# Kernel optimization log

Hardware: AMD Instinct MI355X
Metric: run time of the kernel (lower is better)

## Reference

```python
import jax, jax.numpy as jnp
import numpy as np

BETA = 0.25  # commitment_cost; use_ema=True path -> vq_loss = beta * mse(z_e, sg(z_q))


def setup_inputs() -> dict:
    key = jax.random.key(0)
    k1, k2 = jax.random.split(key)
    B, T, K, D = 8192, 16, 512, 128
    z_e = jax.random.normal(k1, (B, T, D), dtype=jnp.float32)
    # matches nn.init.uniform_(cb.weight, -1/K, 1/K), stacked over T slots
    codebooks = jax.random.uniform(k2, (T, K, D), dtype=jnp.float32,
                                   minval=-1.0 / K, maxval=1.0 / K)
    return {"z_e": z_e, "codebooks": codebooks}


def reference(z_e, codebooks):
    # z_e: (B, T, D); codebooks: (T, K, D)
    B, T, D = z_e.shape
    K = codebooks.shape[1]
    # per-slot squared distances: ||z||^2 - 2 z.w + ||w||^2 -> (B, T, K)
    distances = (jnp.sum(z_e * z_e, axis=-1, keepdims=True)
                 - 2.0 * jnp.einsum('btd,tkd->btk', z_e, codebooks)
                 + jnp.sum(codebooks * codebooks, axis=-1)[None, :, :])
    tokens = jnp.argmin(distances, axis=-1)          # (B, T) int
    # gather per-slot code vectors
    z_q = codebooks[jnp.arange(T)[None, :], tokens]  # (B, T, D)
    # straight-through estimator
    z_q_st = z_e + jax.lax.stop_gradient(z_q - z_e)
    # sum_t beta*mse_t / T == beta * mean over all elements (each slot mse is a B*D mean)
    vq_loss = BETA * jnp.mean(jnp.square(z_e - jax.lax.stop_gradient(z_q)))
    # utilization: total unique codes used per slot / (T*K)
    used = jnp.zeros((T, K), dtype=bool).at[jnp.arange(T)[None, :], tokens].set(True)
    utilization = jnp.sum(used).astype(jnp.float32) / (T * K)
    return z_q_st, tokens, vq_loss, utilization
```

## Files before the change

kernel.cpp:

```cpp
#include <hip/hip_runtime.h>
#include <cfloat>

#define TT 16
#define KK 512
#define DD 128
#define BSTRIPE 512
#define BC 32
#define NW 8
#define NCHUNK (BSTRIPE / BC)
#define N0 16777216
#define N1 131072
#define TAU 1e-4f

typedef _Float16 half8 __attribute__((ext_vector_type(8)));
typedef float f32x16 __attribute__((ext_vector_type(16)));

__device__ __forceinline__ float np_sum128_sq_f4(const float4* __restrict__ p) {
  float4 a = p[0], b = p[1];
  float r[8];
  r[0] = __fmul_rn(a.x, a.x); r[1] = __fmul_rn(a.y, a.y);
  r[2] = __fmul_rn(a.z, a.z); r[3] = __fmul_rn(a.w, a.w);
  r[4] = __fmul_rn(b.x, b.x); r[5] = __fmul_rn(b.y, b.y);
  r[6] = __fmul_rn(b.z, b.z); r[7] = __fmul_rn(b.w, b.w);
#pragma unroll
  for (int i = 1; i < 16; ++i) {
    a = p[2 * i]; b = p[2 * i + 1];
    r[0] = __fadd_rn(r[0], __fmul_rn(a.x, a.x));
    r[1] = __fadd_rn(r[1], __fmul_rn(a.y, a.y));
    r[2] = __fadd_rn(r[2], __fmul_rn(a.z, a.z));
    r[3] = __fadd_rn(r[3], __fmul_rn(a.w, a.w));
    r[4] = __fadd_rn(r[4], __fmul_rn(b.x, b.x));
    r[5] = __fadd_rn(r[5], __fmul_rn(b.y, b.y));
    r[6] = __fadd_rn(r[6], __fmul_rn(b.z, b.z));
    r[7] = __fadd_rn(r[7], __fmul_rn(b.w, b.w));
  }
  return __fadd_rn(__fadd_rn(__fadd_rn(r[0], r[1]), __fadd_rn(r[2], r[3])),
                   __fadd_rn(__fadd_rn(r[4], r[5]), __fadd_rn(r[6], r[7])));
}

__device__ __forceinline__ float dot128_chain(const float* __restrict__ zp,
                                              const float* __restrict__ cp) {
  float s = 0.0f;
#pragma unroll
  for (int d4 = 0; d4 < 32; ++d4) {
    const float4 a = *(const float4*)(zp + d4 * 4);
    const float4 c = *(const float4*)(cp + d4 * 4);
    s = __builtin_fmaf(a.x, c.x, s);
    s = __builtin_fmaf(a.y, c.y, s);
    s = __builtin_fmaf(a.z, c.z, s);
    s = __builtin_fmaf(a.w, c.w, s);
  }
  return s;
}

__device__ __forceinline__ void split8(const float4 a, const float4 b, const float sc,
                                       half8& h1, half8& h2) {
  const float v[8] = {a.x, a.y, a.z, a.w, b.x, b.y, b.z, b.w};
#pragma unroll
  for (int i = 0; i < 8; ++i) {
    const float s = __fmul_rn(v[i], sc);
    const _Float16 p = (_Float16)s;
    const float rr = __fsub_rn(s, (float)p);
    h1[i] = p;
    h2[i] = (_Float16)rr;
  }
}

__device__ __forceinline__ half8 split8_hi(const float4 a, const float4 b, const float sc) {
  const float v[8] = {a.x, a.y, a.z, a.w, b.x, b.y, b.z, b.w};
  half8 h;
#pragma unroll
  for (int i = 0; i < 8; ++i) h[i] = (_Float16)__fmul_rn(v[i], sc);
  return h;
}

__global__ void __launch_bounds__(512, 1)
vq_main(const float* __restrict__ z_e, const float* __restrict__ cb,
        float* __restrict__ out, float* __restrict__ loss_part,
        int* __restrict__ used) {
  __shared__ alignas(16) _Float16 cb2s[KK * DD];
  __shared__ alignas(16) _Float16 zs[BC * 256];
  __shared__ float qs[KK];
  __shared__ float As[BC];
  __shared__ int tok_s[BC];
  __shared__ unsigned long long mrg[BC * NW * 2];
  __shared__ float wred[NW];

  const int tid = threadIdx.x;
  const int t = blockIdx.y;
  const int bbase = blockIdx.x * BSTRIPE;
  const int w = tid >> 6;
  const int lane = tid & 63;
  const int lr = lane & 31;
  const int lhi = lane >> 5;

  {
    const int k = tid;
    const float* src = cb + ((size_t)t * KK + k) * DD;
    float r[8];
    half8 p1, p2;
    {
      const float4 a = *(const float4*)(src);
      const float4 b = *(const float4*)(src + 4);
      r[0] = __fmul_rn(a.x, a.x); r[1] = __fmul_rn(a.y, a.y);
      r[2] = __fmul_rn(a.z, a.z); r[3] = __fmul_rn(a.w, a.w);
      r[4] = __fmul_rn(b.x, b.x); r[5] = __fmul_rn(b.y, b.y);
      r[6] = __fmul_rn(b.z, b.z); r[7] = __fmul_rn(b.w, b.w);
      split8(a, b, 8192.0f, p1, p2);
      *(half8*)(cb2s + k * DD + ((0 ^ (k & 15)) * 8)) = p2;
    }
#pragma unroll
    for (int g = 1; g < 16; ++g) {
      const float4 a = *(const float4*)(src + g * 8);
      const float4 b = *(const float4*)(src + g * 8 + 4);
      r[0] = __fadd_rn(r[0], __fmul_rn(a.x, a.x));
      r[1] = __fadd_rn(r[1], __fmul_rn(a.y, a.y));
      r[2] = __fadd_rn(r[2], __fmul_rn(a.z, a.z));
      r[3] = __fadd_rn(r[3], __fmul_rn(a.w, a.w));
      r[4] = __fadd_rn(r[4], __fmul_rn(b.x, b.x));
      r[5] = __fadd_rn(r[5], __fmul_rn(b.y, b.y));
      r[6] = __fadd_rn(r[6], __fmul_rn(b.z, b.z));
      r[7] = __fadd_rn(r[7], __fmul_rn(b.w, b.w));
      split8(a, b, 8192.0f, p1, p2);
      *(half8*)(cb2s + k * DD + ((g ^ (k & 15)) * 8)) = p2;
    }
    qs[k] = __fadd_rn(__fadd_rn(__fadd_rn(r[0], r[1]), __fadd_rn(r[2], r[3])),
                      __fadd_rn(__fadd_rn(r[4], r[5]), __fadd_rn(r[6], r[7])));
  }

  half8 ca[2][8];
#pragma unroll
  for (int mt = 0; mt < 2; ++mt) {
    const int krow = w * 64 + mt * 32 + lr;
    const float* src = cb + ((size_t)t * KK + krow) * DD + 8 * lhi;
#pragma unroll
    for (int ds = 0; ds < 8; ++ds) {
      const float4 a = *(const float4*)(src + ds * 16);
      const float4 b = *(const float4*)(src + ds * 16 + 4);
      ca[mt][ds] = split8_hi(a, b, 8192.0f);
    }
  }

  float lsum = 0.0f;
  const int srow = tid >> 4, sunit = tid & 15;

  float4 pza, pzb;
  {
    const float* zp = z_e + ((size_t)(bbase + srow) * TT + t) * DD + sunit * 8;
    pza = *(const float4*)zp;
    pzb = *(const float4*)(zp + 4);
  }

#pragma unroll 1
  for (int bc = 0; bc < NCHUNK; ++bc) {
    const int b0 = bbase + bc * BC;
    __syncthreads();

    {
      half8 p1, p2;
      split8(pza, pzb, 128.0f, p1, p2);
      const int c1 = sunit ^ srow;
      const int c2 = (16 + sunit) ^ srow;
      *(half8*)(zs + srow * 256 + c1 * 8) = p1;
      *(half8*)(zs + srow * 256 + c2 * 8) = p2;
      if (tid < BC)
        As[tid] = np_sum128_sq_f4(
            (const float4*)(z_e + ((size_t)(b0 + tid) * TT + t) * DD));
    }
    __syncthreads();

    if (bc + 1 < NCHUNK) {
      const float* zp =
          z_e + ((size_t)(b0 + BC + srow) * TT + t) * DD + sunit * 8;
      pza = *(const float4*)zp;
      pzb = *(const float4*)(zp + 4);
    }

    const float Ab = As[lr];
    unsigned long long b1 = ~0ULL, b2 = ~0ULL;

#pragma unroll 1
    for (int mt = 0; mt < 2; ++mt) {
      f32x16 acc;
#pragma unroll
      for (int i = 0; i < 16; ++i) acc[i] = 0.0f;

#pragma unroll
      for (int ds = 0; ds < 8; ++ds) {
        const int ch = (ds * 2 + lhi) ^ lr;
        const half8 bf = *(const half8*)(zs + lr * 256 + ch * 8);
        acc = __builtin_amdgcn_mfma_f32_32x32x16_f16(ca[mt][ds], bf, acc, 0, 0, 0);
      }
#pragma unroll
      for (int ds = 0; ds < 8; ++ds) {
        const int g = ds * 2 + lhi;
        const int ch = g ^ lr;
        const half8 bf = *(const half8*)(zs + lr * 256 + ch * 8);
        const half8 a2 = *(const half8*)(cb2s + (size_t)(w * 64 + mt * 32 + lr) * DD +
                                         ((g ^ (lr & 15)) * 8));
        acc = __builtin_amdgcn_mfma_f32_32x32x16_f16(a2, bf, acc, 0, 0, 0);
      }
#pragma unroll
      for (int ds = 0; ds < 8; ++ds) {
        const int ch = (16 + ds * 2 + lhi) ^ lr;
        const half8 bf2 = *(const half8*)(zs + lr * 256 + ch * 8);
        acc = __builtin_amdgcn_mfma_f32_32x32x16_f16(ca[mt][ds], bf2, acc, 0, 0, 0);
      }

#pragma unroll
      for (int r = 0; r < 16; ++r) {
        const int k = w * 64 + mt * 32 + (r & 3) + 8 * (r >> 2) + 4 * lhi;
        const float dist =
            __fadd_rn(__fsub_rn(Ab, __fmul_rn(acc[r], 0x1p-19f)), qs[k]);
        const unsigned long long cand =
            ((unsigned long long)__float_as_uint(dist) << 32) | (unsigned)k;
        if (cand < b1) { b2 = b1; b1 = cand; }
        else if (cand < b2) { b2 = cand; }
      }
    }

    {
      const unsigned long long o1 = __shfl_xor(b1, 32, 64);
      const unsigned long long o2 = __shfl_xor(b2, 32, 64);
      const unsigned long long lo = (b1 < o1) ? b1 : o1;
      const unsigned long long hi = (b1 < o1) ? o1 : b1;
      const unsigned long long s2 = (b2 < o2) ? b2 : o2;
      b1 = lo;
      b2 = (hi < s2) ? hi : s2;
    }
    if (lane < 32) {
      mrg[lr * (NW * 2) + w * 2] = b1;
      mrg[lr * (NW * 2) + w * 2 + 1] = b2;
    }
    __syncthreads();

    if ((tid & 15) == 0) {
      const int row = tid >> 4;
      unsigned long long m1 = ~0ULL, m2 = ~0ULL;
#pragma unroll
      for (int g = 0; g < NW * 2; ++g) {
        const unsigned long long v = mrg[row * (NW * 2) + g];
        if (v < m1) { m2 = m1; m1 = v; }
        else if (v < m2) { m2 = v; }
      }
      int tok = (int)(m1 & 0xffffffffULL);
      const float d1f = __uint_as_float((unsigned)(m1 >> 32));
      const float d2f = __uint_as_float((unsigned)(m2 >> 32));
      if (d2f - d1f < TAU) {
        const int k1 = (int)(m1 & 0xffffffffULL);
        const int k2 = (int)(m2 & 0xffffffffULL);
        const float* zp = z_e + ((size_t)(b0 + row) * TT + t) * DD;
        const float Az = As[row];
        const float e1 = dot128_chain(zp, cb + ((size_t)t * KK + k1) * DD);
        const float e2 = dot128_chain(zp, cb + ((size_t)t * KK + k2) * DD);
        const float dd1 = __fadd_rn(__fsub_rn(Az, __fmul_rn(2.0f, e1)), qs[k1]);
        const float dd2 = __fadd_rn(__fsub_rn(Az, __fmul_rn(2.0f, e2)), qs[k2]);
        const unsigned long long c1 =
            ((unsigned long long)__float_as_uint(dd1) << 32) | (unsigned)k1;
        const unsigned long long c2 =
            ((unsigned long long)__float_as_uint(dd2) << 32) | (unsigned)k2;
        tok = (int)(((c1 < c2) ? c1 : c2) & 0xffffffffULL);
      }
      tok_s[row] = tok;
      out[(size_t)N0 + (size_t)(b0 + row) * TT + t] = (float)tok;
      atomicOr(&used[t * KK + tok], 1);
    }
    __syncthreads();

    {
      const int k = tok_s[srow];
      const float* zp = z_e + ((size_t)(b0 + srow) * TT + t) * DD + sunit * 8;
      const float* cp = cb + ((size_t)t * KK + k) * DD + sunit * 8;
      float* op = out + ((size_t)(b0 + srow) * TT + t) * DD + sunit * 8;
#pragma unroll
      for (int h = 0; h < 2; ++h) {
        const float4 zv = *(const float4*)(zp + h * 4);
        const float4 cv = *(const float4*)(cp + h * 4);
        float4 o;
        o.x = __fadd_rn(zv.x, __fsub_rn(cv.x, zv.x));
        o.y = __fadd_rn(zv.y, __fsub_rn(cv.y, zv.y));
        o.z = __fadd_rn(zv.z, __fsub_rn(cv.z, zv.z));
        o.w = __fadd_rn(zv.w, __fsub_rn(cv.w, zv.w));
        *(float4*)(op + h * 4) = o;
        const float dx = zv.x - cv.x, dy = zv.y - cv.y;
        const float dz = zv.z - cv.z, dw = zv.w - cv.w;
        lsum += dx * dx + dy * dy + dz * dz + dw * dw;
      }
    }
  }

#pragma unroll
  for (int off = 32; off > 0; off >>= 1) lsum += __shfl_down(lsum, off, 64);
  if (lane == 0) wred[w] = lsum;
  __syncthreads();
  if (tid == 0) {
    float s = 0.0f;
#pragma unroll
    for (int i = 0; i < NW; ++i) s += wred[i];
    loss_part[blockIdx.y * 16 + blockIdx.x] = s;
  }
}

__global__ void vq_final(const float* __restrict__ loss_part,
                         const int* __restrict__ used, float* __restrict__ out) {
  __shared__ float partf[4];
  __shared__ int   parti[4];
  int tid = threadIdx.x;
  float ls = 0.0f;
  for (int i = tid; i < 256; i += 256) ls += loss_part[i];
  int c = 0;
  for (int i = tid; i < TT * KK; i += 256) c += used[i];
#pragma unroll
  for (int off = 32; off > 0; off >>= 1) {
    ls += __shfl_down(ls, off, 64);
    c  += __shfl_down(c, off, 64);
  }
  if ((tid & 63) == 0) { partf[tid >> 6] = ls; parti[tid >> 6] = c; }
  __syncthreads();
  if (tid == 0) {
    float lt = partf[0] + partf[1] + partf[2] + partf[3];
    int   tot = parti[0] + parti[1] + parti[2] + parti[3];
    out[(size_t)N0 + N1]     = 0.25f * lt / 16777216.0f;
    out[(size_t)N0 + N1 + 1] = (float)tot / 8192.0f;
  }
}

extern "C" void kernel_launch(void* const* d_in, const int* in_sizes, int n_in,
                              void* d_out, int out_size, void* d_ws, size_t ws_size,
                              hipStream_t stream) {
  const float* z_e = (const float*)d_in[0];
  const float* cb  = (const float*)d_in[1];
  float* out = (float*)d_out;
  float* loss_part = (float*)d_ws;
  int*   used      = (int*)((char*)d_ws + 4096);
  hipMemsetAsync(d_ws, 0, 4096 + TT * KK * sizeof(int), stream);
  vq_main<<<dim3(8192 / BSTRIPE, TT), 512, 0, stream>>>(z_e, cb, out, loss_part, used);
  vq_final<<<1, 256, 0, stream>>>(loss_part, used, out);
}
```

Measured before the change: 303.9 us.

## Double wavefronts per block and defer straight-through output to one final pass

Blocks grow from 512 to 1024 threads, and each of the 16 wavefronts now covers 32 codebook rows instead of 64. That halves the per-wave MFMA work and register-resident codebook fragments. The ||z||^2 terms for the whole stripe are computed once up front by the extra threads. Tokens are stored for the whole stripe, and the z_q_st and loss pass moves out of the chunk loop into one sweep at the end, which removes one barrier per chunk. The merge scratch gets an XOR swizzle, at the cost of a deeper 32-entry merge per row and a larger shared-memory footprint.

```diff
diff --git a/kernel.cpp b/kernel.cpp
--- a/kernel.cpp
+++ b/kernel.cpp
@@ -6,7 +6,7 @@
 #define DD 128
 #define BSTRIPE 512
 #define BC 32
-#define NW 8
+#define NW 16
 #define NCHUNK (BSTRIPE / BC)
 #define N0 16777216
 #define N1 131072
@@ -74,16 +74,16 @@
   return h;
 }
 
-__global__ void __launch_bounds__(512, 1)
+__global__ void __launch_bounds__(1024, 1)
 vq_main(const float* __restrict__ z_e, const float* __restrict__ cb,
         float* __restrict__ out, float* __restrict__ loss_part,
         int* __restrict__ used) {
   __shared__ alignas(16) _Float16 cb2s[KK * DD];
   __shared__ alignas(16) _Float16 zs[BC * 256];
   __shared__ float qs[KK];
-  __shared__ float As[BC];
-  __shared__ int tok_s[BC];
-  __shared__ unsigned long long mrg[BC * NW * 2];
+  __shared__ float As_all[BSTRIPE];
+  __shared__ int tok_all[BSTRIPE];
+  __shared__ unsigned long long mrg[BC * (2 * NW)];
   __shared__ float wred[NW];
 
   const int tid = threadIdx.x;
@@ -94,7 +94,7 @@
   const int lr = lane & 31;
   const int lhi = lane >> 5;
 
-  {
+  if (tid < KK) {
     const int k = tid;
     const float* src = cb + ((size_t)t * KK + k) * DD;
     float r[8];
@@ -126,18 +126,21 @@
     }
     qs[k] = __fadd_rn(__fadd_rn(__fadd_rn(r[0], r[1]), __fadd_rn(r[2], r[3])),
                       __fadd_rn(__fadd_rn(r[4], r[5]), __fadd_rn(r[6], r[7])));
-  }
-
-  half8 ca[2][8];
-#pragma unroll
-  for (int mt = 0; mt < 2; ++mt) {
-    const int krow = w * 64 + mt * 32 + lr;
+  } else {
+    const int row = tid - KK;
+    As_all[row] = np_sum128_sq_f4(
+        (const float4*)(z_e + ((size_t)(bbase + row) * TT + t) * DD));
+  }
+
+  half8 ca[8];
+  {
+    const int krow = w * 32 + lr;
     const float* src = cb + ((size_t)t * KK + krow) * DD + 8 * lhi;
 #pragma unroll
     for (int ds = 0; ds < 8; ++ds) {
       const float4 a = *(const float4*)(src + ds * 16);
       const float4 b = *(const float4*)(src + ds * 16 + 4);
-      ca[mt][ds] = split8_hi(a, b, 8192.0f);
+      ca[ds] = split8_hi(a, b, 8192.0f);
     }
   }
 
@@ -145,7 +148,7 @@
   const int srow = tid >> 4, sunit = tid & 15;
 
   float4 pza, pzb;
-  {
+  if (tid < 512) {
     const float* zp = z_e + ((size_t)(bbase + srow) * TT + t) * DD + sunit * 8;
     pza = *(const float4*)zp;
     pzb = *(const float4*)(zp + 4);
@@ -156,69 +159,61 @@
     const int b0 = bbase + bc * BC;
     __syncthreads();
 
-    {
+    if (tid < 512) {
       half8 p1, p2;
       split8(pza, pzb, 128.0f, p1, p2);
       const int c1 = sunit ^ srow;
       const int c2 = (16 + sunit) ^ srow;
       *(half8*)(zs + srow * 256 + c1 * 8) = p1;
       *(half8*)(zs + srow * 256 + c2 * 8) = p2;
-      if (tid < BC)
-        As[tid] = np_sum128_sq_f4(
-            (const float4*)(z_e + ((size_t)(b0 + tid) * TT + t) * DD));
     }
     __syncthreads();
 
-    if (bc + 1 < NCHUNK) {
+    if (tid < 512 && bc + 1 < NCHUNK) {
       const float* zp =
           z_e + ((size_t)(b0 + BC + srow) * TT + t) * DD + sunit * 8;
       pza = *(const float4*)zp;
       pzb = *(const float4*)(zp + 4);
     }
 
-    const float Ab = As[lr];
+    f32x16 acc;
+#pragma unroll
+    for (int i = 0; i < 16; ++i) acc[i] = 0.0f;
+
+#pragma unroll
+    for (int ds = 0; ds < 8; ++ds) {
+      const int ch = (ds * 2 + lhi) ^ lr;
+      const half8 bf = *(const half8*)(zs + lr * 256 + ch * 8);
+      acc = __builtin_amdgcn_mfma_f32_32x32x16_f16(ca[ds], bf, acc, 0, 0, 0);
+    }
+#pragma unroll
+    for (int ds = 0; ds < 8; ++ds) {
+      const int g = ds * 2 + lhi;
+      const int ch = g ^ lr;
+      const half8 bf = *(const half8*)(zs + lr * 256 + ch * 8);
+      const half8 a2 = *(const half8*)(cb2s + (size_t)(w * 32 + lr) * DD +
+                                       ((g ^ (lr & 15)) * 8));
+      acc = __builtin_amdgcn_mfma_f32_32x32x16_f16(a2, bf, acc, 0, 0, 0);
+    }
+#pragma unroll
+    for (int ds = 0; ds < 8; ++ds) {
+      const int ch = (16 + ds * 2 + lhi) ^ lr;
+      const half8 bf2 = *(const half8*)(zs + lr * 256 + ch * 8);
+      acc = __builtin_amdgcn_mfma_f32_32x32x16_f16(ca[ds], bf2, acc, 0, 0, 0);
+    }
+
+    const float Ab = As_all[bc * BC + lr];
     unsigned long long b1 = ~0ULL, b2 = ~0ULL;
-
-#pragma unroll 1
-    for (int mt = 0; mt < 2; ++mt) {
-      f32x16 acc;
-#pragma unroll
-      for (int i = 0; i < 16; ++i) acc[i] = 0.0f;
-
-#pragma unroll
-      for (int ds = 0; ds < 8; ++ds) {
-        const int ch = (ds * 2 + lhi) ^ lr;
-        const half8 bf = *(const half8*)(zs + lr * 256 + ch * 8);
-        acc = __builtin_amdgcn_mfma_f32_32x32x16_f16(ca[mt][ds], bf, acc, 0, 0, 0);
-      }
-#pragma unroll
-      for (int ds = 0; ds < 8; ++ds) {
-        const int g = ds * 2 + lhi;
-        const int ch = g ^ lr;
-        const half8 bf = *(const half8*)(zs + lr * 256 + ch * 8);
-        const half8 a2 = *(const half8*)(cb2s + (size_t)(w * 64 + mt * 32 + lr) * DD +
-                                         ((g ^ (lr & 15)) * 8));
-        acc = __builtin_amdgcn_mfma_f32_32x32x16_f16(a2, bf, acc, 0, 0, 0);
-      }
-#pragma unroll
-      for (int ds = 0; ds < 8; ++ds) {
-        const int ch = (16 + ds * 2 + lhi) ^ lr;
-        const half8 bf2 = *(const half8*)(zs + lr * 256 + ch * 8);
-        acc = __builtin_amdgcn_mfma_f32_32x32x16_f16(ca[mt][ds], bf2, acc, 0, 0, 0);
-      }
-
-#pragma unroll
-      for (int r = 0; r < 16; ++r) {
-        const int k = w * 64 + mt * 32 + (r & 3) + 8 * (r >> 2) + 4 * lhi;
-        const float dist =
-            __fadd_rn(__fsub_rn(Ab, __fmul_rn(acc[r], 0x1p-19f)), qs[k]);
-        const unsigned long long cand =
-            ((unsigned long long)__float_as_uint(dist) << 32) | (unsigned)k;
-        if (cand < b1) { b2 = b1; b1 = cand; }
-        else if (cand < b2) { b2 = cand; }
-      }
-    }
-
+#pragma unroll
+    for (int r = 0; r < 16; ++r) {
+      const int k = w * 32 + (r & 3) + 8 * (r >> 2) + 4 * lhi;
+      const float dist =
+          __fadd_rn(__fsub_rn(Ab, __fmul_rn(acc[r], 0x1p-19f)), qs[k]);
+      const unsigned long long cand =
+          ((unsigned long long)__float_as_uint(dist) << 32) | (unsigned)k;
+      if (cand < b1) { b2 = b1; b1 = cand; }
+      else if (cand < b2) { b2 = cand; }
+    }
     {
       const unsigned long long o1 = __shfl_xor(b1, 32, 64);
       const unsigned long long o2 = __shfl_xor(b2, 32, 64);
@@ -229,17 +224,18 @@
       b2 = (hi < s2) ? hi : s2;
     }
     if (lane < 32) {
-      mrg[lr * (NW * 2) + w * 2] = b1;
-      mrg[lr * (NW * 2) + w * 2 + 1] = b2;
+      const int sl = (w * 2) ^ ((lr & 15) << 1);
+      mrg[lr * (2 * NW) + sl] = b1;
+      mrg[lr * (2 * NW) + sl + 1] = b2;
     }
     __syncthreads();
 
-    if ((tid & 15) == 0) {
-      const int row = tid >> 4;
+    if ((tid & 31) == 0) {
+      const int row = tid >> 5;
       unsigned long long m1 = ~0ULL, m2 = ~0ULL;
 #pragma unroll
-      for (int g = 0; g < NW * 2; ++g) {
-        const unsigned long long v = mrg[row * (NW * 2) + g];
+      for (int g = 0; g < 2 * NW; ++g) {
+        const unsigned long long v = mrg[row * (2 * NW) + g];
         if (v < m1) { m2 = m1; m1 = v; }
         else if (v < m2) { m2 = v; }
       }
@@ -250,7 +246,7 @@
         const int k1 = (int)(m1 & 0xffffffffULL);
         const int k2 = (int)(m2 & 0xffffffffULL);
         const float* zp = z_e + ((size_t)(b0 + row) * TT + t) * DD;
-        const float Az = As[row];
+        const float Az = As_all[bc * BC + row];
         const float e1 = dot128_chain(zp, cb + ((size_t)t * KK + k1) * DD);
         const float e2 = dot128_chain(zp, cb + ((size_t)t * KK + k2) * DD);
         const float dd1 = __fadd_rn(__fsub_rn(Az, __fmul_rn(2.0f, e1)), qs[k1]);
@@ -261,31 +257,34 @@
             ((unsigned long long)__float_as_uint(dd2) << 32) | (unsigned)k2;
         tok = (int)(((c1 < c2) ? c1 : c2) & 0xffffffffULL);
       }
-      tok_s[row] = tok;
+      tok_all[bc * BC + row] = tok;
       out[(size_t)N0 + (size_t)(b0 + row) * TT + t] = (float)tok;
       atomicOr(&used[t * KK + tok], 1);
     }
-    __syncthreads();
-
-    {
-      const int k = tok_s[srow];
-      const float* zp = z_e + ((size_t)(b0 + srow) * TT + t) * DD + sunit * 8;
-      const float* cp = cb + ((size_t)t * KK + k) * DD + sunit * 8;
-      float* op = out + ((size_t)(b0 + srow) * TT + t) * DD + sunit * 8;
-#pragma unroll
-      for (int h = 0; h < 2; ++h) {
-        const float4 zv = *(const float4*)(zp + h * 4);
-        const float4 cv = *(const float4*)(cp + h * 4);
-        float4 o;
-        o.x = __fadd_rn(zv.x, __fsub_rn(cv.x, zv.x));
-        o.y = __fadd_rn(zv.y, __fsub_rn(cv.y, zv.y));
-        o.z = __fadd_rn(zv.z, __fsub_rn(cv.z, zv.z));
-        o.w = __fadd_rn(zv.w, __fsub_rn(cv.w, zv.w));
-        *(float4*)(op + h * 4) = o;
-        const float dx = zv.x - cv.x, dy = zv.y - cv.y;
-        const float dz = zv.z - cv.z, dw = zv.w - cv.w;
-        lsum += dx * dx + dy * dy + dz * dz + dw * dw;
-      }
+  }
+  __syncthreads();
+
+#pragma unroll
+  for (int it = 0; it < 8; ++it) {
+    const int idx = tid + it * 1024;
+    const int row = idx >> 4, unit = idx & 15;
+    const int k = tok_all[row];
+    const float* zp = z_e + ((size_t)(bbase + row) * TT + t) * DD + unit * 8;
+    const float* cp = cb + ((size_t)t * KK + k) * DD + unit * 8;
+    float* op = out + ((size_t)(bbase + row) * TT + t) * DD + unit * 8;
+#pragma unroll
+    for (int h = 0; h < 2; ++h) {
+      const float4 zv = *(const float4*)(zp + h * 4);
+      const float4 cv = *(const float4*)(cp + h * 4);
+      float4 o;
+      o.x = __fadd_rn(zv.x, __fsub_rn(cv.x, zv.x));
+      o.y = __fadd_rn(zv.y, __fsub_rn(cv.y, zv.y));
+      o.z = __fadd_rn(zv.z, __fsub_rn(cv.z, zv.z));
+      o.w = __fadd_rn(zv.w, __fsub_rn(cv.w, zv.w));
+      *(float4*)(op + h * 4) = o;
+      const float dx = zv.x - cv.x, dy = zv.y - cv.y;
+      const float dz = zv.z - cv.z, dw = zv.w - cv.w;
+      lsum += dx * dx + dy * dy + dz * dz + dw * dw;
     }
   }
 
@@ -334,6 +333,6 @@
   float* loss_part = (float*)d_ws;
   int*   used      = (int*)((char*)d_ws + 4096);
   hipMemsetAsync(d_ws, 0, 4096 + TT * KK * sizeof(int), stream);
-  vq_main<<<dim3(8192 / BSTRIPE, TT), 512, 0, stream>>>(z_e, cb, out, loss_part, used);
+  vq_main<<<dim3(8192 / BSTRIPE, TT), 1024, 0, stream>>>(z_e, cb, out, loss_part, used);
   vq_final<<<1, 256, 0, stream>>>(loss_part, used, out);
 }
```

Measured after the change: 457.4 us. 50.5% more time.
